# Kernel tuning notes

Hardware: AMD Instinct MI355X
Metric: run time of the kernel (lower is better)

The kernel has to match this reference:

```python
import jax, jax.numpy as jnp
import numpy as np

N, D_IN, D_HID, N_EXPERTS, TOP_K = 16384, 2048, 2048, 8, 2


def setup_inputs() -> dict:
    key = jax.random.key(0)
    k1, k2, k3, k4, k5 = jax.random.split(key, 5)
    x = jax.random.normal(k1, (N, D_IN), dtype=jnp.float32)
    W_experts = jax.random.normal(k2, (N_EXPERTS, D_IN, D_HID), dtype=jnp.float32) * 0.02
    b_experts = jax.random.normal(k3, (N_EXPERTS, D_HID), dtype=jnp.float32) * 0.02
    W_gate = jax.random.normal(k4, (D_IN, N_EXPERTS), dtype=jnp.float32) * 0.02
    b_gate = jax.random.normal(k5, (N_EXPERTS,), dtype=jnp.float32) * 0.02
    return {"x": x, "W_experts": W_experts, "b_experts": b_experts,
            "W_gate": W_gate, "b_gate": b_gate}


def reference(x, W_experts, b_experts, W_gate, b_gate):
    # gating softmax over experts: [N, E]
    gates = jax.nn.softmax(x @ W_gate + b_gate, axis=-1)
    # per-token top-k scores/indices: [N, K]
    top_scores, top_idx = jax.lax.top_k(gates, TOP_K)
    # FAITHFUL to original: experts chosen by the FIRST token's indices for all tokens
    idx0 = top_idx[0]                       # [K]
    W_sel = W_experts[idx0]                 # [K, D_IN, D_HID]
    b_sel = b_experts[idx0]                 # [K, D_HID]
    expert_out = jnp.einsum('ni,kio->nko', x, W_sel) + b_sel[None]  # [N, K, D_HID]
    # weight by each token's own top-k scores and sum over the K experts
    return (expert_out * top_scores[:, :, None]).sum(axis=1)        # [N, D_HID]
```

## Files before the change

kernel.cpp:

```cpp
#include <hip/hip_runtime.h>
#include <hip/hip_bf16.h>
#include <stdint.h>

#define N_TOK 16384
#define D_IN  2048
#define D_HID 2048

typedef __attribute__((ext_vector_type(8))) short  bf16x8;
typedef __attribute__((ext_vector_type(4))) float  f32x4;
typedef __attribute__((ext_vector_type(8))) unsigned short u16x8;

__device__ __forceinline__ unsigned short f2bf(float f) {
    unsigned int u = __float_as_uint(f);
    u = (u + 0x7FFFu + ((u >> 16) & 1u)) >> 16;
    return (unsigned short)u;
}

__global__ __launch_bounds__(256) void xconv3_kernel(
    const float* __restrict__ x, const float* __restrict__ Wg,
    unsigned short* __restrict__ xb, float* __restrict__ part) {
    const int mt = blockIdx.x >> 3;
    const int g  = blockIdx.x & 7;
    const int t  = threadIdx.x;

    float p[8];
#pragma unroll
    for (int e = 0; e < 8; ++e) p[e] = 0.f;

#pragma unroll
    for (int q = 0; q < 8; ++q) {
        const int kt = g * 8 + q;
        const float* src = x + ((size_t)(mt * 256 + t)) * D_IN + kt * 32;
        unsigned short* slab = xb + ((size_t)(mt * 64 + kt)) * 8192;
        const float* wg = Wg + kt * 32 * 8;
#pragma unroll
        for (int ks = 0; ks < 4; ++ks) {
            float4 a = *(const float4*)(src + ks * 8);
            float4 b = *(const float4*)(src + ks * 8 + 4);
            float xv[8] = {a.x, a.y, a.z, a.w, b.x, b.y, b.z, b.w};
            u16x8 v;
#pragma unroll
            for (int j = 0; j < 8; ++j) v[j] = f2bf(xv[j]);
            *(u16x8*)(slab + (ks * 256 + t) * 8) = v;
#pragma unroll
            for (int j = 0; j < 8; ++j)
#pragma unroll
                for (int e = 0; e < 8; ++e)
                    p[e] += xv[j] * wg[(ks * 8 + j) * 8 + e];
        }
    }
    float* dst = part + (((size_t)(mt * 8 + g)) * 256 + t) * 8;
#pragma unroll
    for (int e = 0; e < 8; ++e) dst[e] = p[e];
}

__global__ __launch_bounds__(256) void gatefin_kernel(
    const float* __restrict__ part, const float* __restrict__ bg,
    float* __restrict__ s12, int* __restrict__ eidx) {
    __shared__ float red[4][64][8];
    const int mt  = blockIdx.x >> 2;
    const int q   = blockIdx.x & 3;
    const int tok = threadIdx.x & 63;
    const int s   = threadIdx.x >> 6;

    float l8[8];
#pragma unroll
    for (int e = 0; e < 8; ++e) l8[e] = 0.f;
#pragma unroll
    for (int gg = 0; gg < 2; ++gg) {
        const int gidx = s * 2 + gg;
        const float* pp =
            part + (((size_t)(mt * 8 + gidx)) * 256 + q * 64 + tok) * 8;
        float4 a = *(const float4*)pp;
        float4 b = *(const float4*)(pp + 4);
        l8[0] += a.x; l8[1] += a.y; l8[2] += a.z; l8[3] += a.w;
        l8[4] += b.x; l8[5] += b.y; l8[6] += b.z; l8[7] += b.w;
    }
#pragma unroll
    for (int e = 0; e < 8; ++e) red[s][tok][e] = l8[e];
    __syncthreads();
    if (s == 0) {
        float mx = -1e30f;
#pragma unroll
        for (int e = 0; e < 8; ++e) {
            l8[e] = red[0][tok][e] + red[1][tok][e] + red[2][tok][e] +
                    red[3][tok][e] + bg[e];
            mx = fmaxf(mx, l8[e]);
        }
        float sum = 0.f;
#pragma unroll
        for (int e = 0; e < 8; ++e) { l8[e] = expf(l8[e] - mx); sum += l8[e]; }
        float inv = 1.f / sum;
        float s1 = -1.f, s2 = -1.f; int i1 = 0, i2 = 0;
#pragma unroll
        for (int e = 0; e < 8; ++e) {
            float g = l8[e] * inv;
            if (g > s1)      { s2 = s1; i2 = i1; s1 = g; i1 = e; }
            else if (g > s2) { s2 = g;  i2 = e; }
        }
        const int token = mt * 256 + q * 64 + tok;
        s12[token * 2]     = s1;
        s12[token * 2 + 1] = s2;
        if (token == 0) { eidx[0] = i1; eidx[1] = i2; }
    }
}

__global__ void wconv_kernel(const float* __restrict__ W,
                             const int* __restrict__ eidx,
                             unsigned short* __restrict__ wbT) {
    __shared__ float tile[64][65];
    const int be  = blockIdx.z;
    const int e   = eidx[be];
    const int k0  = blockIdx.y * 64;
    const int n0  = blockIdx.x * 64;
    const int bx  = n0 >> 7;
    const int cl0 = n0 & 127;
    const int kt0 = k0 >> 5;
    const float* src = W + (size_t)e * D_IN * D_HID;
    const int t = threadIdx.x;

#pragma unroll
    for (int p = 0; p < 4; ++p) {
        int row = p * 16 + (t >> 4);
        int col = (t & 15) * 4;
        const float* s = src + (size_t)(k0 + row) * D_HID + n0 + col;
        tile[row][col]     = s[0];
        tile[row][col + 1] = s[1];
        tile[row][col + 2] = s[2];
        tile[row][col + 3] = s[3];
    }
    __syncthreads();

    const int g   = (t >> 5) * 8;
    const int ktl = t >> 7;
    const int ks  = (t >> 5) & 3;
#pragma unroll
    for (int p = 0; p < 2; ++p) {
        int n = p * 32 + (t & 31);
        u16x8 v;
#pragma unroll
        for (int j = 0; j < 8; ++j) v[j] = f2bf(tile[g + j][n]);
        unsigned short* dst = wbT + ((size_t)(bx * 64 + kt0 + ktl)) * 8192 +
                              ((size_t)(ks * 256 + be * 128 + cl0 + n)) * 8;
        *(u16x8*)dst = v;
    }
}

#define GLD16(gp, lp)                                                        \
    __builtin_amdgcn_global_load_lds(                                        \
        (const __attribute__((address_space(1))) void*)(gp),                 \
        (__attribute__((address_space(3))) void*)(lp), 16, 0, 0)

#define LDSV(SLOT) (*(const bf16x8*)&lds[(SLOT) * 8])

#define STAGE_A(SBAS, KT)                                                    \
    do {                                                                     \
        GLD16(gA0 + (size_t)(KT) * 8192,        &lds[((SBAS) + t512) * 8]);  \
        GLD16(gA0 + (size_t)(KT) * 8192 + 4096, &lds[((SBAS) + 512 + t512) * 8]); \
    } while (0)
#define STAGE_B(SBAS, KT)                                                    \
    do {                                                                     \
        GLD16(gB0 + (size_t)(KT) * 8192,        &lds[((SBAS) + 1024 + t512) * 8]); \
        GLD16(gB0 + (size_t)(KT) * 8192 + 4096, &lds[((SBAS) + 1536 + t512) * 8]); \
    } while (0)

#define MF(MI, AV)                                                                              \
    acc[MI][0] = __builtin_amdgcn_mfma_f32_16x16x32_bf16(AV, bf0, acc[MI][0], 0, 0, 0);         \
    acc[MI][1] = __builtin_amdgcn_mfma_f32_16x16x32_bf16(AV, bf1, acc[MI][1], 0, 0, 0);         \
    acc[MI][2] = __builtin_amdgcn_mfma_f32_16x16x32_bf16(AV, bf2, acc[MI][2], 0, 0, 0);         \
    acc[MI][3] = __builtin_amdgcn_mfma_f32_16x16x32_bf16(AV, bf3, acc[MI][3], 0, 0, 0);

#define TILE(RB, SB, KT, DO_STAGE, VMSTR)                                    \
    do {                                                                     \
        const int rbas  = (RB) * 2048;                                       \
        const int abase = rbas + aks + arow;                                 \
        const int bbase = rbas + 1024 + aks + brow;                          \
        bf16x8 bf0 = LDSV(bbase), bf1 = LDSV(bbase + 16),                    \
               bf2 = LDSV(bbase + 32), bf3 = LDSV(bbase + 48);               \
        bf16x8 a0 = LDSV(abase), a1 = LDSV(abase + 16),                      \
               a2 = LDSV(abase + 32), a3 = LDSV(abase + 48);                 \
        bf16x8 a4 = LDSV(abase + 64), a5 = LDSV(abase + 80),                 \
               a6 = LDSV(abase + 96), a7 = LDSV(abase + 112);                \
        if (DO_STAGE) { STAGE_A((SB) * 2048, KT); STAGE_B((SB) * 2048, KT); }\
        if (VMSTR[0]) asm volatile(VMSTR ::: "memory");                      \
        __builtin_amdgcn_s_barrier();                                        \
        __builtin_amdgcn_s_setprio(1);                                       \
        MF(0, a0) MF(1, a1) MF(2, a2) MF(3, a3)                              \
        MF(4, a4) MF(5, a5) MF(6, a6) MF(7, a7)                              \
        __builtin_amdgcn_s_setprio(0);                                       \
    } while (0)

__global__ __launch_bounds__(512, 2) void moe_gemm_kernel(
    const unsigned short* __restrict__ xb,
    const unsigned short* __restrict__ wbT,
    const float* __restrict__ b_exp,
    const int* __restrict__ eidx,
    const float* __restrict__ s12,
    float* __restrict__ out) {
    __shared__ __align__(16) short lds[4 * 2048 * 8];

    const int t512 = threadIdx.x;
    const int lane = t512 & 63;
    const int w    = t512 >> 6;
    const int wm   = w >> 2;
    const int wn   = w & 3;

    const int bid = blockIdx.x;
    const int xcd = bid & 7;
    const int jb  = bid >> 3;
    const int bx  = xcd * 2 + (jb & 1);
    const int by  = jb >> 1;
    const int mbase = by * 256;
    const int nbase = bx * 128;

    const unsigned short* gA0 = xb  + ((size_t)by * 64) * 8192 + t512 * 8;
    const unsigned short* gB0 = wbT + ((size_t)bx * 64) * 8192 + t512 * 8;

    const int aks  = (lane >> 4) * 256;
    const int arow = wm * 128 + (lane & 15);
    const int brow = wn * 64 + (lane & 15);

    f32x4 acc[8][4];
#pragma unroll
    for (int mi = 0; mi < 8; ++mi)
#pragma unroll
        for (int ni = 0; ni < 4; ++ni) acc[mi][ni] = (f32x4){0.f, 0.f, 0.f, 0.f};

    STAGE_A(0, 0);    STAGE_B(0, 0);
    STAGE_A(2048, 1); STAGE_B(2048, 1);
    STAGE_A(4096, 2); STAGE_B(4096, 2);
    asm volatile("s_waitcnt vmcnt(4)" ::: "memory");
    __builtin_amdgcn_s_barrier();

#pragma unroll 4
    for (int t = 0; t < 61; ++t) {
        TILE(t & 3, (t + 3) & 3, t + 3, 1, "s_waitcnt vmcnt(4)");
    }
    TILE(1, 0, 0, 0, "s_waitcnt vmcnt(4)");
    TILE(2, 0, 0, 0, "s_waitcnt vmcnt(0)");
    TILE(3, 0, 0, 0, "");

    __syncthreads();
    float* fl = (float*)lds;
    if (wn >= 2) {
        float* reg = fl + (wm * 2 + (wn - 2)) * 8192;
#pragma unroll
        for (int mi = 0; mi < 8; ++mi)
#pragma unroll
            for (int ni = 0; ni < 4; ++ni)
#pragma unroll
                for (int j = 0; j < 4; ++j) {
                    int row_l = mi * 16 + ((lane >> 4) << 2) + j;
                    int col_l = ni * 16 + (lane & 15);
                    reg[row_l * 64 + col_l] = acc[mi][ni][j];
                }
    }
    __syncthreads();
    if (wn < 2) {
        const float* reg = fl + (wm * 2 + wn) * 8192;
        const int e0 = eidx[0], e1 = eidx[1];
        const float* bb0 = b_exp + (size_t)e0 * D_HID;
        const float* bb1 = b_exp + (size_t)e1 * D_HID;
        const float2* s12v = (const float2*)s12;
        int   cc[4];
        float b0c[4], b1c[4];
#pragma unroll
        for (int ni = 0; ni < 4; ++ni) {
            cc[ni]  = nbase + wn * 64 + ni * 16 + (lane & 15);
            b0c[ni] = bb0[cc[ni]];
            b1c[ni] = bb1[cc[ni]];
        }
#pragma unroll
        for (int mi = 0; mi < 8; ++mi)
#pragma unroll
            for (int j = 0; j < 4; ++j) {
                int row_l = mi * 16 + ((lane >> 4) << 2) + j;
                int r = mbase + wm * 128 + row_l;
                float2 s = s12v[r];
#pragma unroll
                for (int ni = 0; ni < 4; ++ni) {
                    float y1 = reg[row_l * 64 + ni * 16 + (lane & 15)];
                    out[(size_t)r * D_HID + cc[ni]] =
                        s.x * (acc[mi][ni][j] + b0c[ni]) + s.y * (y1 + b1c[ni]);
                }
            }
    }
}

extern "C" void kernel_launch(void* const* d_in, const int* in_sizes, int n_in,
                              void* d_out, int out_size, void* d_ws, size_t ws_size,
                              hipStream_t stream) {
    const float* x         = (const float*)d_in[0];
    const float* W_experts = (const float*)d_in[1];
    const float* b_experts = (const float*)d_in[2];
    const float* W_gate    = (const float*)d_in[3];
    const float* b_gate    = (const float*)d_in[4];
    float* out = (float*)d_out;

    char* ws = (char*)d_ws;
    float* s12  = (float*)ws;
    int*   eidx = (int*)(ws + 131072);
    unsigned short* xb  = (unsigned short*)(ws + 262144);
    unsigned short* wbT = (unsigned short*)(ws + 262144 + 67108864);
    float* part = out;

    xconv3_kernel<<<512, 256, 0, stream>>>(x, W_gate, xb, part);
    gatefin_kernel<<<256, 256, 0, stream>>>(part, b_gate, s12, eidx);
    wconv_kernel<<<dim3(32, 32, 2), 256, 0, stream>>>(W_experts, eidx, wbT);
    moe_gemm_kernel<<<1024, 512, 0, stream>>>(xb, wbT, b_experts, eidx, s12, out);
}
```

Baseline: 291.7 us.

## Compute token-0 expert choice upfront and merge x/W conversion into one launch

A tiny single-wave kernel computes the gate logits for token 0 and picks its top-2 experts before anything else runs. The x conversion with partial gate sums and the selected-expert weight transposition then run as one combined grid, so they can overlap instead of being serialized behind the gate finalize kernel. Top-2 is taken on logits instead of softmax probabilities, which gives the same order since softmax is monotonic. The cost is an extra small serial launch with almost no parallelism, and the combined kernel now reserves the tile shared memory for every block, including the x-conversion blocks that do not use it.

```diff
diff --git a/kernel.cpp b/kernel.cpp
--- a/kernel.cpp
+++ b/kernel.cpp
@@ -16,47 +16,122 @@
     return (unsigned short)u;
 }
 
-__global__ __launch_bounds__(256) void xconv3_kernel(
+__global__ void gate0_kernel(const float* __restrict__ x,
+                             const float* __restrict__ Wg,
+                             const float* __restrict__ bg,
+                             int* __restrict__ eidx) {
+    const int lane = threadIdx.x;
+    float acc[8];
+#pragma unroll
+    for (int e = 0; e < 8; ++e) acc[e] = 0.f;
+    for (int i = lane; i < D_IN; i += 64) {
+        float xv = x[i];
+        const float4* wr = (const float4*)(Wg + (size_t)i * 8);
+        float4 w0 = wr[0], w1 = wr[1];
+        acc[0] += xv * w0.x; acc[1] += xv * w0.y;
+        acc[2] += xv * w0.z; acc[3] += xv * w0.w;
+        acc[4] += xv * w1.x; acc[5] += xv * w1.y;
+        acc[6] += xv * w1.z; acc[7] += xv * w1.w;
+    }
+#pragma unroll
+    for (int off = 32; off > 0; off >>= 1)
+#pragma unroll
+        for (int e = 0; e < 8; ++e) acc[e] += __shfl_xor(acc[e], off);
+    if (lane == 0) {
+        float s1 = -1e30f, s2 = -1e30f; int i1 = 0, i2 = 0;
+#pragma unroll
+        for (int e = 0; e < 8; ++e) {
+            float g = acc[e] + bg[e];
+            if (g > s1)      { s2 = s1; i2 = i1; s1 = g; i1 = e; }
+            else if (g > s2) { s2 = g;  i2 = e; }
+        }
+        eidx[0] = i1; eidx[1] = i2;
+    }
+}
+
+__global__ __launch_bounds__(256) void prep_kernel(
     const float* __restrict__ x, const float* __restrict__ Wg,
-    unsigned short* __restrict__ xb, float* __restrict__ part) {
-    const int mt = blockIdx.x >> 3;
-    const int g  = blockIdx.x & 7;
-    const int t  = threadIdx.x;
-
-    float p[8];
-#pragma unroll
-    for (int e = 0; e < 8; ++e) p[e] = 0.f;
-
-#pragma unroll
-    for (int q = 0; q < 8; ++q) {
-        const int kt = g * 8 + q;
-        const float* src = x + ((size_t)(mt * 256 + t)) * D_IN + kt * 32;
-        unsigned short* slab = xb + ((size_t)(mt * 64 + kt)) * 8192;
-        const float* wg = Wg + kt * 32 * 8;
-#pragma unroll
-        for (int ks = 0; ks < 4; ++ks) {
-            float4 a = *(const float4*)(src + ks * 8);
-            float4 b = *(const float4*)(src + ks * 8 + 4);
-            float xv[8] = {a.x, a.y, a.z, a.w, b.x, b.y, b.z, b.w};
-            u16x8 v;
-#pragma unroll
-            for (int j = 0; j < 8; ++j) v[j] = f2bf(xv[j]);
-            *(u16x8*)(slab + (ks * 256 + t) * 8) = v;
-#pragma unroll
-            for (int j = 0; j < 8; ++j)
-#pragma unroll
-                for (int e = 0; e < 8; ++e)
-                    p[e] += xv[j] * wg[(ks * 8 + j) * 8 + e];
-        }
-    }
-    float* dst = part + (((size_t)(mt * 8 + g)) * 256 + t) * 8;
-#pragma unroll
-    for (int e = 0; e < 8; ++e) dst[e] = p[e];
+    const float* __restrict__ W, const int* __restrict__ eidx,
+    unsigned short* __restrict__ xb, float* __restrict__ part,
+    unsigned short* __restrict__ wbT) {
+    __shared__ float tile[64][65];
+    const int bid = blockIdx.x;
+    const int t   = threadIdx.x;
+    if (bid < 512) {
+        const int mt = bid >> 3;
+        const int g  = bid & 7;
+        float p[8];
+#pragma unroll
+        for (int e = 0; e < 8; ++e) p[e] = 0.f;
+#pragma unroll
+        for (int q = 0; q < 8; ++q) {
+            const int kt = g * 8 + q;
+            const float* src = x + ((size_t)(mt * 256 + t)) * D_IN + kt * 32;
+            unsigned short* slab = xb + ((size_t)(mt * 64 + kt)) * 8192;
+            const float* wg = Wg + kt * 32 * 8;
+#pragma unroll
+            for (int ks = 0; ks < 4; ++ks) {
+                float4 a = *(const float4*)(src + ks * 8);
+                float4 b = *(const float4*)(src + ks * 8 + 4);
+                float xv[8] = {a.x, a.y, a.z, a.w, b.x, b.y, b.z, b.w};
+                u16x8 v;
+#pragma unroll
+                for (int j = 0; j < 8; ++j) v[j] = f2bf(xv[j]);
+                *(u16x8*)(slab + (ks * 256 + t) * 8) = v;
+#pragma unroll
+                for (int j = 0; j < 8; ++j)
+#pragma unroll
+                    for (int e = 0; e < 8; ++e)
+                        p[e] += xv[j] * wg[(ks * 8 + j) * 8 + e];
+            }
+        }
+        float* dst = part + (((size_t)(mt * 8 + g)) * 256 + t) * 8;
+#pragma unroll
+        for (int e = 0; e < 8; ++e) dst[e] = p[e];
+        return;
+    }
+    const int bid2 = bid - 512;
+    const int nx   = bid2 & 31;
+    const int ky   = (bid2 >> 5) & 31;
+    const int be   = bid2 >> 10;
+    const int e    = eidx[be];
+    const int k0   = ky * 64;
+    const int n0   = nx * 64;
+    const int bx   = n0 >> 7;
+    const int cl0  = n0 & 127;
+    const int kt0  = k0 >> 5;
+    const float* src = W + (size_t)e * D_IN * D_HID;
+
+#pragma unroll
+    for (int p = 0; p < 4; ++p) {
+        int row = p * 16 + (t >> 4);
+        int col = (t & 15) * 4;
+        const float* s = src + (size_t)(k0 + row) * D_HID + n0 + col;
+        tile[row][col]     = s[0];
+        tile[row][col + 1] = s[1];
+        tile[row][col + 2] = s[2];
+        tile[row][col + 3] = s[3];
+    }
+    __syncthreads();
+
+    const int g   = (t >> 5) * 8;
+    const int ktl = t >> 7;
+    const int ks  = (t >> 5) & 3;
+#pragma unroll
+    for (int p = 0; p < 2; ++p) {
+        int n = p * 32 + (t & 31);
+        u16x8 v;
+#pragma unroll
+        for (int j = 0; j < 8; ++j) v[j] = f2bf(tile[g + j][n]);
+        unsigned short* dst = wbT + ((size_t)(bx * 64 + kt0 + ktl)) * 8192 +
+                              ((size_t)(ks * 256 + be * 128 + cl0 + n)) * 8;
+        *(u16x8*)dst = v;
+    }
 }
 
 __global__ __launch_bounds__(256) void gatefin_kernel(
     const float* __restrict__ part, const float* __restrict__ bg,
-    float* __restrict__ s12, int* __restrict__ eidx) {
+    float* __restrict__ s12) {
     __shared__ float red[4][64][8];
     const int mt  = blockIdx.x >> 2;
     const int q   = blockIdx.x & 3;
@@ -91,58 +166,16 @@
 #pragma unroll
         for (int e = 0; e < 8; ++e) { l8[e] = expf(l8[e] - mx); sum += l8[e]; }
         float inv = 1.f / sum;
-        float s1 = -1.f, s2 = -1.f; int i1 = 0, i2 = 0;
+        float s1 = -1.f, s2 = -1.f;
 #pragma unroll
         for (int e = 0; e < 8; ++e) {
             float g = l8[e] * inv;
-            if (g > s1)      { s2 = s1; i2 = i1; s1 = g; i1 = e; }
-            else if (g > s2) { s2 = g;  i2 = e; }
+            if (g > s1)      { s2 = s1; s1 = g; }
+            else if (g > s2) { s2 = g; }
         }
         const int token = mt * 256 + q * 64 + tok;
         s12[token * 2]     = s1;
         s12[token * 2 + 1] = s2;
-        if (token == 0) { eidx[0] = i1; eidx[1] = i2; }
-    }
-}
-
-__global__ void wconv_kernel(const float* __restrict__ W,
-                             const int* __restrict__ eidx,
-                             unsigned short* __restrict__ wbT) {
-    __shared__ float tile[64][65];
-    const int be  = blockIdx.z;
-    const int e   = eidx[be];
-    const int k0  = blockIdx.y * 64;
-    const int n0  = blockIdx.x * 64;
-    const int bx  = n0 >> 7;
-    const int cl0 = n0 & 127;
-    const int kt0 = k0 >> 5;
-    const float* src = W + (size_t)e * D_IN * D_HID;
-    const int t = threadIdx.x;
-
-#pragma unroll
-    for (int p = 0; p < 4; ++p) {
-        int row = p * 16 + (t >> 4);
-        int col = (t & 15) * 4;
-        const float* s = src + (size_t)(k0 + row) * D_HID + n0 + col;
-        tile[row][col]     = s[0];
-        tile[row][col + 1] = s[1];
-        tile[row][col + 2] = s[2];
-        tile[row][col + 3] = s[3];
-    }
-    __syncthreads();
-
-    const int g   = (t >> 5) * 8;
-    const int ktl = t >> 7;
-    const int ks  = (t >> 5) & 3;
-#pragma unroll
-    for (int p = 0; p < 2; ++p) {
-        int n = p * 32 + (t & 31);
-        u16x8 v;
-#pragma unroll
-        for (int j = 0; j < 8; ++j) v[j] = f2bf(tile[g + j][n]);
-        unsigned short* dst = wbT + ((size_t)(bx * 64 + kt0 + ktl)) * 8192 +
-                              ((size_t)(ks * 256 + be * 128 + cl0 + n)) * 8;
-        *(u16x8*)dst = v;
     }
 }
 
@@ -304,8 +337,9 @@
     unsigned short* wbT = (unsigned short*)(ws + 262144 + 67108864);
     float* part = out;
 
-    xconv3_kernel<<<512, 256, 0, stream>>>(x, W_gate, xb, part);
-    gatefin_kernel<<<256, 256, 0, stream>>>(part, b_gate, s12, eidx);
-    wconv_kernel<<<dim3(32, 32, 2), 256, 0, stream>>>(W_experts, eidx, wbT);
+    gate0_kernel<<<1, 64, 0, stream>>>(x, W_gate, b_gate, eidx);
+    prep_kernel<<<2560, 256, 0, stream>>>(x, W_gate, W_experts, eidx,
+                                          xb, part, wbT);
+    gatefin_kernel<<<256, 256, 0, stream>>>(part, b_gate, s12);
     moe_gemm_kernel<<<1024, 512, 0, stream>>>(xb, wbT, b_experts, eidx, s12, out);
 }
```

Result: slower. 300.9 us (+3.2%).
